# Optimization experiments

Measured on AMD Instinct MI355X. Metric: run time of the kernel, lower is better.

## Reference

```python
import jax, jax.numpy as jnp
import numpy as np

BN_EPS = 1e-5


def _gcn_norm(edge_index, n):
    # PyG gcn_norm with add_self_loops=True: deg counts in-degree incl. self loop
    loops = jnp.arange(n, dtype=edge_index.dtype)
    src = jnp.concatenate([edge_index[0], loops])
    dst = jnp.concatenate([edge_index[1], loops])
    deg = jax.ops.segment_sum(jnp.ones(src.shape[0], jnp.float32), dst, num_segments=n)
    dinv = jnp.where(deg > 0, jax.lax.rsqrt(jnp.maximum(deg, 1.0)), 0.0)
    norm = dinv[src] * dinv[dst]  # [E + N]
    return src, dst, norm


def _gcn_conv(x, src, dst, norm, W, b, n):
    h = x @ W                      # dense transform first (fewer FLOPs: d_out gather)
    msgs = h[src] * norm[:, None]  # [E+N, d_out] gathered, degree-normalized
    return jax.ops.segment_sum(msgs, dst, num_segments=n) + b


def _bn_relu(x, gamma, beta):
    # BatchNorm1d in training mode: biased batch stats over node dim
    mu = x.mean(axis=0)
    var = x.var(axis=0)
    return jax.nn.relu(gamma * (x - mu) * jax.lax.rsqrt(var + BN_EPS) + beta)


def setup_inputs() -> dict:
    key = jax.random.key(0)
    ks = jax.random.split(key, 8)
    N, E, D_IN, H1, H2, D_OUT = 50000, 500000, 128, 256, 512, 128
    x = jax.random.normal(ks[0], (N, D_IN), jnp.float32)
    edge_index = jax.random.randint(ks[1], (2, E), 0, N, jnp.int64)
    def lin(k, fan_in, fan_out):
        bound = 1.0 / np.sqrt(fan_in)
        kw, kb = jax.random.split(k)
        W = jax.random.uniform(kw, (fan_in, fan_out), jnp.float32, -bound, bound)
        b = jax.random.uniform(kb, (fan_out,), jnp.float32, -bound, bound)
        return W, b
    W1, b1 = lin(ks[2], D_IN, H1)
    W2, b2 = lin(ks[3], H1, H2)
    Wl, bl = lin(ks[4], H2, D_OUT)
    return {
        "x": x, "edge_index": edge_index,
        "W1": W1, "b1": b1, "gamma1": jnp.ones((H1,), jnp.float32), "beta1": jnp.zeros((H1,), jnp.float32),
        "W2": W2, "b2": b2, "gamma2": jnp.ones((H2,), jnp.float32), "beta2": jnp.zeros((H2,), jnp.float32),
        "Wl": Wl, "bl": bl,
    }


def reference(x, edge_index, W1, b1, gamma1, beta1, W2, b2, gamma2, beta2, Wl, bl):
    n = x.shape[0]
    src, dst, norm = _gcn_norm(edge_index, n)
    h = _bn_relu(_gcn_conv(x, src, dst, norm, W1, b1, n), gamma1, beta1)
    h = _bn_relu(_gcn_conv(h, src, dst, norm, W2, b2, n), gamma2, beta2)
    return h @ Wl + bl
```

## Files before the change

### kernel.cpp

```cpp
#include <hip/hip_runtime.h>
#include <cstdint>
#include <cstddef>

typedef __bf16 bf16;
typedef bf16 bf16x2 __attribute__((ext_vector_type(2)));
typedef bf16 bf16x4 __attribute__((ext_vector_type(4)));
typedef bf16 bf16x8 __attribute__((ext_vector_type(8)));
typedef float f32x4 __attribute__((ext_vector_type(4)));

__global__ void k_init(int* __restrict__ deg, int* __restrict__ cur,
                       float* __restrict__ sums1, float* __restrict__ sums2, int N) {
  int i = blockIdx.x * 256 + threadIdx.x;
  if (i < N) { deg[i] = 1; cur[i] = 0; }
  if (i < 512)  sums1[i] = 0.f;
  if (i < 1024) sums2[i] = 0.f;
}

__global__ void k_count(const int* __restrict__ ei, int* __restrict__ deg, int E) {
  int e = blockIdx.x * 256 + threadIdx.x;
  if (e < E) atomicAdd(&deg[ei[E + e]], 1);
}

__global__ __launch_bounds__(256) void k_scan1(const int* __restrict__ deg,
                                               int* __restrict__ bsum, int N) {
  int t = threadIdx.x;
  int i = blockIdx.x * 256 + t;
  int v = (i < N) ? deg[i] - 1 : 0;
#pragma unroll
  for (int off = 32; off > 0; off >>= 1) v += __shfl_down(v, off, 64);
  __shared__ int red[4];
  if ((t & 63) == 0) red[t >> 6] = v;
  __syncthreads();
  if (t == 0) bsum[blockIdx.x] = red[0] + red[1] + red[2] + red[3];
}

__global__ __launch_bounds__(256) void k_scan2(const int* __restrict__ bsum,
                                               int* __restrict__ bpre, int B) {
  __shared__ int s[256];
  int t = threadIdx.x;
  int v = (t < B) ? bsum[t] : 0;
  s[t] = v;
  __syncthreads();
  for (int off = 1; off < 256; off <<= 1) {
    int add = (t >= off) ? s[t - off] : 0;
    __syncthreads();
    s[t] += add;
    __syncthreads();
  }
  if (t < B) bpre[t] = s[t] - v;
}

__global__ __launch_bounds__(256) void k_scan3(const int* __restrict__ deg,
                                               const int* __restrict__ bpre,
                                               int* __restrict__ roff,
                                               float* __restrict__ dinv, int N) {
  __shared__ int s[256];
  int t = threadIdx.x;
  int i = blockIdx.x * 256 + t;
  int d = (i < N) ? deg[i] : 1;
  int v = d - 1;
  if (i >= N) v = 0;
  s[t] = v;
  __syncthreads();
  for (int off = 1; off < 256; off <<= 1) {
    int add = (t >= off) ? s[t - off] : 0;
    __syncthreads();
    s[t] += add;
    __syncthreads();
  }
  if (i < N) {
    int base = bpre[blockIdx.x];
    roff[i] = base + s[t] - v;
    dinv[i] = rsqrtf((float)d);
    if (i == N - 1) roff[N] = base + s[t];
  }
}

__global__ void k_scatter(const int* __restrict__ ei, const int* __restrict__ roff,
                          int* __restrict__ cur, int* __restrict__ csr, int E) {
  int e = blockIdx.x * 256 + threadIdx.x;
  if (e >= E) return;
  int d = ei[E + e];
  int p = atomicAdd(&cur[d], 1);
  csr[roff[d] + p] = ei[e];
}

__global__ void k_cvt_x(const float* __restrict__ x, bf16* __restrict__ xb, size_t total) {
  size_t base = ((size_t)blockIdx.x * 256 + threadIdx.x) * 4;
  if (base >= total) return;
  const float4 v = *(const float4*)(x + base);
  bf16x4 o;
  o[0] = (bf16)v.x; o[1] = (bf16)v.y; o[2] = (bf16)v.z; o[3] = (bf16)v.w;
  *(bf16x4*)(xb + base) = o;
}

__global__ void k_cvt_w(const float* __restrict__ W1, const float* __restrict__ W2,
                        const float* __restrict__ Wl, bf16* __restrict__ w1t,
                        bf16* __restrict__ w2t, bf16* __restrict__ wlt) {
  int i = blockIdx.x * 256 + threadIdx.x;
  if (i < 32768) {
    int n = i >> 7, k = i & 127;
    w1t[i] = (bf16)W1[(size_t)k * 256 + n];
  } else if (i < 163840) {
    int j = i - 32768;
    int n = j >> 8, k = j & 255;
    w2t[j] = (bf16)W2[(size_t)k * 512 + n];
  } else {
    int j = i - 163840;
    int n = j >> 9, k = j & 511;
    wlt[j] = (bf16)Wl[(size_t)k * 128 + n];
  }
}

template<int K, int NOUT, bool FINAL>
__global__ __launch_bounds__(256) void k_gemm(const bf16* __restrict__ A,
                                              const bf16* __restrict__ Bt,
                                              bf16* __restrict__ outB,
                                              float* __restrict__ outF,
                                              const float* __restrict__ bias,
                                              float* __restrict__ sums,
                                              int Mreal) {
  __shared__ uint4 lA[512];
  __shared__ uint4 lB[512];
  const int tid = threadIdx.x;
  const int wv = tid >> 6, lane = tid & 63;
  const int q = lane >> 4, mr = lane & 15;
  const int m0 = blockIdx.x * 128;
  const int n0 = blockIdx.y * 128;
  const int rw = (wv >> 1) * 64, cw = (wv & 1) * 64;
  f32x4 acc[4][4];
#pragma unroll
  for (int r = 0; r < 4; ++r)
#pragma unroll
    for (int c = 0; c < 4; ++c) acc[r][c] = (f32x4){0.f, 0.f, 0.f, 0.f};

  for (int k0 = 0; k0 < K; k0 += 32) {
    __syncthreads();
#pragma unroll
    for (int it = 0; it < 2; ++it) {
      int s = it * 256 + tid;
      int row = s & 127, kb = s >> 7;
      const bf16* ga = A + (size_t)(m0 + row) * K + (k0 + kb * 8);
      const bf16* gb = Bt + (size_t)(n0 + row) * K + (k0 + kb * 8);
      __builtin_amdgcn_global_load_lds((const __attribute__((address_space(1))) void*)ga,
                                       (__attribute__((address_space(3))) void*)(lA + s), 16, 0, 0);
      __builtin_amdgcn_global_load_lds((const __attribute__((address_space(1))) void*)gb,
                                       (__attribute__((address_space(3))) void*)(lB + s), 16, 0, 0);
    }
    __syncthreads();
    bf16x8 af[4], bfr[4];
#pragma unroll
    for (int r = 0; r < 4; ++r)
      af[r] = ((const bf16x8*)lA)[q * 128 + rw + r * 16 + mr];
#pragma unroll
    for (int c = 0; c < 4; ++c)
      bfr[c] = ((const bf16x8*)lB)[q * 128 + cw + c * 16 + mr];
#pragma unroll
    for (int r = 0; r < 4; ++r)
#pragma unroll
      for (int c = 0; c < 4; ++c)
        acc[r][c] = __builtin_amdgcn_mfma_f32_16x16x32_bf16(af[r], bfr[c], acc[r][c], 0, 0, 0);
  }

#pragma unroll
  for (int c = 0; c < 4; ++c) {
    const int col = n0 + cw + c * 16 + mr;
    float s0 = 0.f, s1 = 0.f;
#pragma unroll
    for (int r = 0; r < 4; ++r) {
#pragma unroll
      for (int i = 0; i < 4; ++i) {
        int row = m0 + rw + r * 16 + q * 4 + i;
        float v = acc[r][c][i];
        if (FINAL) {
          if (row < Mreal) outF[(size_t)row * NOUT + col] = v + bias[col];
        } else {
          outB[(size_t)row * NOUT + col] = (bf16)v;
          if (row < Mreal) { s0 += v; s1 += v * v; }
        }
      }
    }
    if (!FINAL) {
      s0 += __shfl_xor(s0, 16, 64); s0 += __shfl_xor(s0, 32, 64);
      s1 += __shfl_xor(s1, 16, 64); s1 += __shfl_xor(s1, 32, 64);
      if (q == 0) { atomicAdd(&sums[col], s0); atomicAdd(&sums[NOUT + col], s1); }
    }
  }
}

template<int C, bool BN>
__global__ __launch_bounds__(256) void k_agg(const bf16* __restrict__ h,
                                             bf16* __restrict__ g,
                                             const int* __restrict__ csr,
                                             const int* __restrict__ roff,
                                             const float* __restrict__ dinv,
                                             const float* __restrict__ scale,
                                             const float* __restrict__ shift,
                                             int N) {
  constexpr int VPL = C / 64;
  const int lane = threadIdx.x & 63;
  const int v = (int)(((unsigned)blockIdx.x * 256 + threadIdx.x) >> 6);
  if (v >= N) return;
  float sc[VPL], sh[VPL];
  if constexpr (BN) {
#pragma unroll
    for (int u = 0; u < VPL; ++u) { sc[u] = scale[lane * VPL + u]; sh[u] = shift[lane * VPL + u]; }
  }
  const float dv = dinv[v];
  float acc[VPL];
#pragma unroll
  for (int u = 0; u < VPL; ++u) acc[u] = 0.f;

  auto accum = [&](int src, float w) {
    const bf16* hr = h + (size_t)src * C + lane * VPL;
    float vals[VPL];
    if constexpr (VPL == 2) {
      bf16x2 t = *(const bf16x2*)hr;
      vals[0] = (float)t[0]; vals[1] = (float)t[1];
    } else {
      bf16x4 t = *(const bf16x4*)hr;
#pragma unroll
      for (int u = 0; u < 4; ++u) vals[u] = (float)t[u];
    }
#pragma unroll
    for (int u = 0; u < VPL; ++u) {
      float xx = vals[u];
      if constexpr (BN) xx = fmaxf(0.f, xx * sc[u] + sh[u]);
      acc[u] += w * xx;
    }
  };

  accum(v, dv);
  const int beg = roff[v], end = roff[v + 1];
  for (int base = beg; base < end; base += 64) {
    int cnt = min(64, end - base);
    int s = 0; float w = 0.f;
    if (lane < cnt) { s = csr[base + lane]; w = dinv[s]; }
    for (int j = 0; j < cnt; ++j) {
      int sj = __shfl(s, j, 64);
      float wj = __shfl(w, j, 64);
      accum(sj, wj);
    }
  }

  bf16* gv = g + (size_t)v * C + lane * VPL;
  if constexpr (VPL == 2) {
    bf16x2 o;
    o[0] = (bf16)(acc[0] * dv); o[1] = (bf16)(acc[1] * dv);
    *(bf16x2*)gv = o;
  } else {
    bf16x4 o;
#pragma unroll
    for (int u = 0; u < 4; ++u) o[u] = (bf16)(acc[u] * dv);
    *(bf16x4*)gv = o;
  }
}

__global__ void k_bnfinal(const float* __restrict__ sums, const float* __restrict__ gamma,
                          const float* __restrict__ beta, float* __restrict__ scale,
                          float* __restrict__ shift, int C, float invN) {
  int c = blockIdx.x * 256 + threadIdx.x;
  if (c >= C) return;
  float mu = sums[c] * invN;
  float var = sums[C + c] * invN - mu * mu;
  float is = rsqrtf(var + 1e-5f);
  float sc = gamma[c] * is;
  scale[c] = sc;
  shift[c] = beta[c] - mu * sc;
}

template<int C>
__global__ void k_bnapply(bf16* __restrict__ g, const float* __restrict__ scale,
                          const float* __restrict__ shift, size_t total) {
  size_t base = ((size_t)blockIdx.x * 256 + threadIdx.x) * 8;
  if (base >= total) return;
  int col = (int)(base & (size_t)(C - 1));
  bf16x8 t = *(const bf16x8*)(g + base);
  bf16x8 o;
#pragma unroll
  for (int j = 0; j < 8; ++j)
    o[j] = (bf16)fmaxf(0.f, (float)t[j] * scale[col + j] + shift[col + j]);
  *(bf16x8*)(g + base) = o;
}

extern "C" void kernel_launch(void* const* d_in, const int* in_sizes, int n_in,
                              void* d_out, int out_size, void* d_ws, size_t ws_size,
                              hipStream_t stream) {
  const float* x   = (const float*)d_in[0];
  const int*   ei  = (const int*)d_in[1];
  const float* W1  = (const float*)d_in[2];
  const float* g1  = (const float*)d_in[4];
  const float* be1 = (const float*)d_in[5];
  const float* W2  = (const float*)d_in[6];
  const float* g2  = (const float*)d_in[8];
  const float* be2 = (const float*)d_in[9];
  const float* Wl  = (const float*)d_in[10];
  const float* bl  = (const float*)d_in[11];
  float* out = (float*)d_out;

  const int N  = in_sizes[0] / 128;
  const int E  = in_sizes[1] / 2;
  const int Mp = ((N + 127) / 128) * 128;
  const int NB = (N + 255) / 256;

  char* p = (char*)d_ws;
  auto carve = [&](size_t bytes) { void* r = (void*)p; p += (bytes + 255) & ~(size_t)255; return r; };
  int*   deg   = (int*)carve(sizeof(int) * N);
  int*   cur   = (int*)carve(sizeof(int) * N);
  int*   roff  = (int*)carve(sizeof(int) * (N + 1));
  int*   csr   = (int*)carve(sizeof(int) * E);
  int*   bsum  = (int*)carve(sizeof(int) * 256);
  int*   bpre  = (int*)carve(sizeof(int) * 256);
  float* dinv  = (float*)carve(sizeof(float) * N);
  float* sums1 = (float*)carve(sizeof(float) * 512);
  float* sums2 = (float*)carve(sizeof(float) * 1024);
  float* sc1   = (float*)carve(sizeof(float) * 256);
  float* sh1   = (float*)carve(sizeof(float) * 256);
  float* sc2   = (float*)carve(sizeof(float) * 512);
  float* sh2   = (float*)carve(sizeof(float) * 512);
  bf16*  w1t   = (bf16*)carve(sizeof(bf16) * 256 * 128);
  bf16*  w2t   = (bf16*)carve(sizeof(bf16) * 512 * 256);
  bf16*  wlt   = (bf16*)carve(sizeof(bf16) * 128 * 512);
  bf16*  xb    = (bf16*)carve(sizeof(bf16) * (size_t)Mp * 128);
  bf16*  ax1   = (bf16*)carve(sizeof(bf16) * (size_t)Mp * 128);
  bf16*  t1    = (bf16*)carve(sizeof(bf16) * (size_t)Mp * 256);
  bf16*  ax2   = (bf16*)carve(sizeof(bf16) * (size_t)Mp * 256);
  bf16*  t2    = (bf16*)carve(sizeof(bf16) * (size_t)Mp * 512);
  (void)n_in; (void)out_size; (void)ws_size;

  const int gE = (E + 255) / 256;
  k_init<<<NB, 256, 0, stream>>>(deg, cur, sums1, sums2, N);
  k_count<<<gE, 256, 0, stream>>>(ei, deg, E);
  k_scan1<<<NB, 256, 0, stream>>>(deg, bsum, N);
  k_scan2<<<1, 256, 0, stream>>>(bsum, bpre, NB);
  k_scan3<<<NB, 256, 0, stream>>>(deg, bpre, roff, dinv, N);
  k_scatter<<<gE, 256, 0, stream>>>(ei, roff, cur, csr, E);

  k_cvt_x<<<(int)(((size_t)N * 128 / 4 + 255) / 256), 256, 0, stream>>>(x, xb, (size_t)N * 128);
  k_cvt_w<<<896, 256, 0, stream>>>(W1, W2, Wl, w1t, w2t, wlt);

  const int gAgg = (N + 3) / 4;
  k_agg<128, false><<<gAgg, 256, 0, stream>>>(xb, ax1, csr, roff, dinv, nullptr, nullptr, N);
  k_gemm<128, 256, false><<<dim3(Mp / 128, 2), 256, 0, stream>>>(ax1, w1t, t1, nullptr, nullptr, sums1, N);
  k_bnfinal<<<1, 256, 0, stream>>>(sums1, g1, be1, sc1, sh1, 256, 1.f / (float)N);

  k_agg<256, true><<<gAgg, 256, 0, stream>>>(t1, ax2, csr, roff, dinv, sc1, sh1, N);
  k_gemm<256, 512, false><<<dim3(Mp / 128, 4), 256, 0, stream>>>(ax2, w2t, t2, nullptr, nullptr, sums2, N);
  k_bnfinal<<<2, 256, 0, stream>>>(sums2, g2, be2, sc2, sh2, 512, 1.f / (float)N);
  k_bnapply<512><<<(int)(((size_t)Mp * 512 / 8 + 255) / 256), 256, 0, stream>>>(t2, sc2, sh2, (size_t)Mp * 512);

  k_gemm<512, 128, true><<<dim3(Mp / 128, 1), 256, 0, stream>>>(t2, wlt, nullptr, out, bl, nullptr, N);
}
```

Measured before the change: 403.9 us.

## Permute GEMM output channels for packed bf16x4 stores and reorder grid

The GEMM epilogue now writes each lane's four column fragments as one packed bf16x4 store instead of scalar bf16 stores. This stores the intermediate activations in a permuted channel order. The permutation is undone by permuting the K rows of the next layer's transposed weights and by looking up gamma/beta through the inverse map in the BN finalize step. The launch grid is also swapped so N-tiles vary fastest, letting blocks that share the same A rows run close together for better cache reuse. The cost is extra index arithmetic and a tightly coupled layout convention across kernels.

```diff
diff --git a/kernel.cpp b/kernel.cpp
--- a/kernel.cpp
+++ b/kernel.cpp
@@ -7,6 +7,10 @@
 typedef bf16 bf16x4 __attribute__((ext_vector_type(4)));
 typedef bf16 bf16x8 __attribute__((ext_vector_type(8)));
 typedef float f32x4 __attribute__((ext_vector_type(4)));
+
+__device__ __forceinline__ int perm_src(int s) {
+  return (s & ~63) | ((s & 3) << 4) | ((s & 63) >> 2);
+}
 
 __global__ void k_init(int* __restrict__ deg, int* __restrict__ cur,
                        float* __restrict__ sums1, float* __restrict__ sums2, int N) {
@@ -103,12 +107,12 @@
     w1t[i] = (bf16)W1[(size_t)k * 256 + n];
   } else if (i < 163840) {
     int j = i - 32768;
-    int n = j >> 8, k = j & 255;
-    w2t[j] = (bf16)W2[(size_t)k * 512 + n];
+    int n = j >> 8, ks = j & 255;
+    w2t[j] = (bf16)W2[(size_t)perm_src(ks) * 512 + n];
   } else {
     int j = i - 163840;
-    int n = j >> 9, k = j & 511;
-    wlt[j] = (bf16)Wl[(size_t)k * 128 + n];
+    int n = j >> 9, ks = j & 511;
+    wlt[j] = (bf16)Wl[(size_t)perm_src(ks) * 128 + n];
   }
 }
 
@@ -125,8 +129,8 @@
   const int tid = threadIdx.x;
   const int wv = tid >> 6, lane = tid & 63;
   const int q = lane >> 4, mr = lane & 15;
-  const int m0 = blockIdx.x * 128;
-  const int n0 = blockIdx.y * 128;
+  const int n0 = blockIdx.x * 128;
+  const int m0 = blockIdx.y * 128;
   const int rw = (wv >> 1) * 64, cw = (wv & 1) * 64;
   f32x4 acc[4][4];
 #pragma unroll
@@ -162,28 +166,49 @@
         acc[r][c] = __builtin_amdgcn_mfma_f32_16x16x32_bf16(af[r], bfr[c], acc[r][c], 0, 0, 0);
   }
 
-#pragma unroll
-  for (int c = 0; c < 4; ++c) {
-    const int col = n0 + cw + c * 16 + mr;
-    float s0 = 0.f, s1 = 0.f;
+  if (FINAL) {
+#pragma unroll
+    for (int c = 0; c < 4; ++c) {
+      const int col = n0 + cw + c * 16 + mr;
+#pragma unroll
+      for (int r = 0; r < 4; ++r) {
+#pragma unroll
+        for (int i = 0; i < 4; ++i) {
+          int row = m0 + rw + r * 16 + q * 4 + i;
+          if (row < Mreal) outF[(size_t)row * NOUT + col] = acc[r][c][i] + bias[col];
+        }
+      }
+    }
+  } else {
 #pragma unroll
     for (int r = 0; r < 4; ++r) {
 #pragma unroll
       for (int i = 0; i < 4; ++i) {
         int row = m0 + rw + r * 16 + q * 4 + i;
-        float v = acc[r][c][i];
-        if (FINAL) {
-          if (row < Mreal) outF[(size_t)row * NOUT + col] = v + bias[col];
-        } else {
-          outB[(size_t)row * NOUT + col] = (bf16)v;
+        bf16x4 pk;
+        pk[0] = (bf16)acc[r][0][i]; pk[1] = (bf16)acc[r][1][i];
+        pk[2] = (bf16)acc[r][2][i]; pk[3] = (bf16)acc[r][3][i];
+        *(bf16x4*)(outB + (size_t)row * NOUT + n0 + cw + mr * 4) = pk;
+      }
+    }
+#pragma unroll
+    for (int c = 0; c < 4; ++c) {
+      float s0 = 0.f, s1 = 0.f;
+#pragma unroll
+      for (int r = 0; r < 4; ++r) {
+#pragma unroll
+        for (int i = 0; i < 4; ++i) {
+          int row = m0 + rw + r * 16 + q * 4 + i;
+          float v = acc[r][c][i];
           if (row < Mreal) { s0 += v; s1 += v * v; }
         }
       }
-    }
-    if (!FINAL) {
       s0 += __shfl_xor(s0, 16, 64); s0 += __shfl_xor(s0, 32, 64);
       s1 += __shfl_xor(s1, 16, 64); s1 += __shfl_xor(s1, 32, 64);
-      if (q == 0) { atomicAdd(&sums[col], s0); atomicAdd(&sums[NOUT + col], s1); }
+      if (q == 0) {
+        int sch = n0 + cw + mr * 4 + c;
+        atomicAdd(&sums[sch], s0); atomicAdd(&sums[NOUT + sch], s1);
+      }
     }
   }
 }
@@ -261,12 +286,13 @@
                           float* __restrict__ shift, int C, float invN) {
   int c = blockIdx.x * 256 + threadIdx.x;
   if (c >= C) return;
+  int src = perm_src(c);
   float mu = sums[c] * invN;
   float var = sums[C + c] * invN - mu * mu;
   float is = rsqrtf(var + 1e-5f);
-  float sc = gamma[c] * is;
+  float sc = gamma[src] * is;
   scale[c] = sc;
-  shift[c] = beta[c] - mu * sc;
+  shift[c] = beta[src] - mu * sc;
 }
 
 template<int C>
@@ -341,13 +367,13 @@
 
   const int gAgg = (N + 3) / 4;
   k_agg<128, false><<<gAgg, 256, 0, stream>>>(xb, ax1, csr, roff, dinv, nullptr, nullptr, N);
-  k_gemm<128, 256, false><<<dim3(Mp / 128, 2), 256, 0, stream>>>(ax1, w1t, t1, nullptr, nullptr, sums1, N);
+  k_gemm<128, 256, false><<<dim3(2, Mp / 128), 256, 0, stream>>>(ax1, w1t, t1, nullptr, nullptr, sums1, N);
   k_bnfinal<<<1, 256, 0, stream>>>(sums1, g1, be1, sc1, sh1, 256, 1.f / (float)N);
 
   k_agg<256, true><<<gAgg, 256, 0, stream>>>(t1, ax2, csr, roff, dinv, sc1, sh1, N);
-  k_gemm<256, 512, false><<<dim3(Mp / 128, 4), 256, 0, stream>>>(ax2, w2t, t2, nullptr, nullptr, sums2, N);
+  k_gemm<256, 512, false><<<dim3(4, Mp / 128), 256, 0, stream>>>(ax2, w2t, t2, nullptr, nullptr, sums2, N);
   k_bnfinal<<<2, 256, 0, stream>>>(sums2, g2, be2, sc2, sh2, 512, 1.f / (float)N);
   k_bnapply<512><<<(int)(((size_t)Mp * 512 / 8 + 255) / 256), 256, 0, stream>>>(t2, sc2, sh2, (size_t)Mp * 512);
 
-  k_gemm<512, 128, true><<<dim3(Mp / 128, 1), 256, 0, stream>>>(t2, wlt, nullptr, out, bl, nullptr, N);
-}
+  k_gemm<512, 128, true><<<dim3(1, Mp / 128), 256, 0, stream>>>(t2, wlt, nullptr, out, bl, nullptr, N);
+}
```

After: 475.7 us. 1.18x slower.
